# Performance work log

Hardware: AMD Instinct MI355X
Metric: run time of the kernel (lower is better)

The kernel has to match this reference:

```python
import jax, jax.numpy as jnp
import numpy as np

N_NODES = 1_000_000
N_EDGES = 4_000_000  # knn_k = 4
N_GRAPHS = 1024
HIDDEN = 64
N_FEAT = 4


def setup_inputs() -> dict:
    key = jax.random.key(0)
    k0, k1, k2, k3, k4 = jax.random.split(key, 5)
    x = jax.random.normal(k0, (N_NODES, N_FEAT), dtype=jnp.float32)
    edge_index = jax.random.randint(k1, (2, N_EDGES), 0, N_NODES, dtype=jnp.int64)
    batch = jnp.sort(jax.random.randint(k2, (N_NODES,), 0, N_GRAPHS, dtype=jnp.int64))
    W1 = jax.random.normal(k3, (N_FEAT, HIDDEN), dtype=jnp.float32) * 0.5
    b1 = jnp.zeros((HIDDEN,), dtype=jnp.float32)
    W2 = jax.random.normal(k4, (HIDDEN, 1), dtype=jnp.float32) * 0.1
    b2 = jnp.zeros((1,), dtype=jnp.float32)
    return {"x": x, "W1": W1, "b1": b1, "W2": W2, "b2": b2,
            "edge_index": edge_index, "batch": batch}


def gcn_conv(x, edge_index, W, b):
    # PyG GCNConv: linear transform, add self-loops, sym-normalize, scatter-add.
    n = x.shape[0]
    h = x @ W  # [N, 64]
    loop = jnp.arange(n, dtype=edge_index.dtype)
    row = jnp.concatenate([edge_index[0], loop])  # source j
    col = jnp.concatenate([edge_index[1], loop])  # target i
    deg = jax.ops.segment_sum(jnp.ones_like(col, dtype=h.dtype), col, num_segments=n)
    dis = jnp.where(deg > 0, jax.lax.rsqrt(jnp.maximum(deg, 1.0)), 0.0)
    norm = dis[row] * dis[col]  # [E+N]
    out = jax.ops.segment_sum(h[row] * norm[:, None], col, num_segments=n)
    return out + b


def reference(x, W1, b1, W2, b2, edge_index, batch):
    h = gcn_conv(x, edge_index, W1, b1)          # [N, 64]
    h = jax.nn.elu(h)                            # ELU activation
    pooled = jax.ops.segment_sum(h, batch, num_segments=N_GRAPHS)  # global_add_pool
    return pooled @ W2 + b2                      # [G, 1]
```

## Files before the change

kernel.cpp:

```cpp
#include <hip/hip_runtime.h>
#include <hip/hip_fp16.h>

#define N_NODES 1000000
#define N_EDGES 4000000
#define N_GRAPHS 1024
#define HIDDEN 64

#define G1 250
#define T1 512
#define EPB (N_EDGES / G1)
#define EPB4 (EPB / 4)
#define BSHIFT 10
#define BSIZE 1024
#define NBK 1024
#define NBUCK ((N_NODES + BSIZE - 1) / BSIZE)

typedef int   vi4 __attribute__((ext_vector_type(4)));
typedef unsigned vu4 __attribute__((ext_vector_type(4)));
typedef float vf4 __attribute__((ext_vector_type(4)));

__device__ __forceinline__ int4 nt_int4(const int4* p) {
    vi4 v = __builtin_nontemporal_load((const vi4*)p);
    return make_int4(v.x, v.y, v.z, v.w);
}
__device__ __forceinline__ uint4 nt_uint4(const uint4* p) {
    vu4 v = __builtin_nontemporal_load((const vu4*)p);
    return make_uint4(v.x, v.y, v.z, v.w);
}
__device__ __forceinline__ float4 nt_float4(const float4* p) {
    vf4 v = __builtin_nontemporal_load((const vf4*)p);
    return make_float4(v.x, v.y, v.z, v.w);
}

__global__ __launch_bounds__(T1) void k_hist(const int4* __restrict__ col4,
                                             int* __restrict__ part,
                                             float* __restrict__ out,
                                             const float* __restrict__ b2) {
    __shared__ int h[NBK];
    int t = threadIdx.x, blk = blockIdx.x;
    for (int i = t; i < NBK; i += T1) h[i] = 0;
    int gid = blk * T1 + t;
    if (gid < N_GRAPHS) out[gid] = b2[0];
    __syncthreads();
    int b0 = blk * EPB4;
    for (int i = t; i < EPB4; i += T1) {
        int4 c = nt_int4(col4 + b0 + i);
        atomicAdd(&h[((unsigned)c.x) >> BSHIFT], 1);
        atomicAdd(&h[((unsigned)c.y) >> BSHIFT], 1);
        atomicAdd(&h[((unsigned)c.z) >> BSHIFT], 1);
        atomicAdd(&h[((unsigned)c.w) >> BSHIFT], 1);
    }
    __syncthreads();
    for (int i = t; i < NBK; i += T1) part[blk * NBK + i] = h[i];
}

__global__ __launch_bounds__(256) void k_colscan(int* __restrict__ part,
                                                 int* __restrict__ ecnt) {
    int b = blockIdx.x;
    int t = threadIdx.x;
    __shared__ int a[256];
    int v = (t < G1) ? part[t * NBK + b] : 0;
    a[t] = v;
    __syncthreads();
    for (int o = 1; o < 256; o <<= 1) {
        int u = (t >= o) ? a[t - o] : 0;
        __syncthreads();
        a[t] += u;
        __syncthreads();
    }
    if (t < G1) part[t * NBK + b] = a[t] - v;
    if (t == 255) ecnt[b] = a[255];
}

__global__ __launch_bounds__(NBK) void k_bscan(const int* __restrict__ ecnt,
                                               int* __restrict__ ebase) {
    __shared__ int sc[NBK];
    int b = threadIdx.x;
    int run4 = (ecnt[b] + 3) & ~3;
    sc[b] = run4;
    __syncthreads();
    for (int o = 1; o < NBK; o <<= 1) {
        int v = (b >= o) ? sc[b - o] : 0;
        __syncthreads();
        sc[b] += v;
        __syncthreads();
    }
    ebase[b] = sc[b] - run4;
}

__global__ __launch_bounds__(T1) void k_part(const int4* __restrict__ row4,
                                             const int4* __restrict__ col4,
                                             const int* __restrict__ part,
                                             const int* __restrict__ ebase,
                                             unsigned* __restrict__ epair) {
    __shared__ int cur[NBK];
    int t = threadIdx.x, blk = blockIdx.x;
    for (int i = t; i < NBK; i += T1) cur[i] = part[blk * NBK + i] + ebase[i];
    __syncthreads();
    int b0 = blk * EPB4;
    for (int i = t; i < EPB4; i += T1) {
        int4 c = nt_int4(col4 + b0 + i);
        int4 r = nt_int4(row4 + b0 + i);
        int cc[4] = {c.x, c.y, c.z, c.w};
        int rr[4] = {r.x, r.y, r.z, r.w};
        #pragma unroll
        for (int k = 0; k < 4; ++k) {
            int b = ((unsigned)cc[k]) >> BSHIFT;
            int pos = atomicAdd(&cur[b], 1);
            epair[pos] = ((unsigned)(cc[k] & (BSIZE - 1)) << 20) | (unsigned)rr[k];
        }
    }
}

__global__ __launch_bounds__(512) void k_deg2(const unsigned* __restrict__ epair,
                                              const int* __restrict__ ebase,
                                              const int* __restrict__ ecnt,
                                              const float4* __restrict__ x,
                                              float* __restrict__ dis,
                                              uint2* __restrict__ xdh) {
    __shared__ int deg[BSIZE];
    int t = threadIdx.x, b = blockIdx.x;
    for (int i = t; i < BSIZE; i += 512) deg[i] = 1;
    __syncthreads();
    int ne = ecnt[b];
    const unsigned* ep = epair + ebase[b];
    int ne4 = ne & ~3;
    for (int i = 4 * t; i < ne4; i += 2048) {
        uint4 u = nt_uint4((const uint4*)(ep + i));
        atomicAdd(&deg[u.x >> 20], 1);
        atomicAdd(&deg[u.y >> 20], 1);
        atomicAdd(&deg[u.z >> 20], 1);
        atomicAdd(&deg[u.w >> 20], 1);
    }
    for (int i = ne4 + t; i < ne; i += 512) atomicAdd(&deg[ep[i] >> 20], 1);
    __syncthreads();
    int n0 = b << BSHIFT;
    for (int i = t; i < BSIZE; i += 512) {
        int node = n0 + i;
        if (node < N_NODES) {
            float d = rsqrtf((float)deg[i]);
            dis[node] = d;
            float4 xv = nt_float4(x + node);
            __half2 h01 = __floats2half2_rn(xv.x * d, xv.y * d);
            __half2 h23 = __floats2half2_rn(xv.z * d, xv.w * d);
            uint2 pk;
            pk.x = *(unsigned*)&h01;
            pk.y = *(unsigned*)&h23;
            xdh[node] = pk;
        }
    }
}

__device__ __forceinline__ void acc_edge(unsigned u, uint2 p, float* sf) {
    int loc = u >> 20;
    __half2 h01 = *(__half2*)&p.x;
    __half2 h23 = *(__half2*)&p.y;
    float2 f01 = __half22float2(h01);
    float2 f23 = __half22float2(h23);
    float* sp = sf + loc * 5;
    atomicAdd(sp + 0, f01.x);
    atomicAdd(sp + 1, f01.y);
    atomicAdd(sp + 2, f23.x);
    atomicAdd(sp + 3, f23.y);
}

__global__ __launch_bounds__(512) void k_accF(const unsigned* __restrict__ epair,
                                              const int* __restrict__ ebase,
                                              const int* __restrict__ ecnt,
                                              const uint2* __restrict__ xdh,
                                              const float* __restrict__ dis,
                                              const int* __restrict__ batch,
                                              const float* __restrict__ W1,
                                              const float* __restrict__ b1,
                                              const float* __restrict__ W2,
                                              float* __restrict__ out) {
    __shared__ float sf[BSIZE * 5];
    int t = threadIdx.x, b = blockIdx.x;
    for (int i = t; i < BSIZE * 5; i += 512) sf[i] = 0.f;
    __syncthreads();
    int ne = ecnt[b];
    const unsigned* ep = epair + ebase[b];
    int ne8 = ne & ~7;
    for (int i = 8 * t; i < ne8; i += 4096) {
        uint4 q0 = nt_uint4((const uint4*)(ep + i));
        uint4 q1 = nt_uint4((const uint4*)(ep + i + 4));
        uint2 p0 = xdh[q0.x & 0xFFFFFu];
        uint2 p1 = xdh[q0.y & 0xFFFFFu];
        uint2 p2 = xdh[q0.z & 0xFFFFFu];
        uint2 p3 = xdh[q0.w & 0xFFFFFu];
        uint2 p4 = xdh[q1.x & 0xFFFFFu];
        uint2 p5 = xdh[q1.y & 0xFFFFFu];
        uint2 p6 = xdh[q1.z & 0xFFFFFu];
        uint2 p7 = xdh[q1.w & 0xFFFFFu];
        acc_edge(q0.x, p0, sf);
        acc_edge(q0.y, p1, sf);
        acc_edge(q0.z, p2, sf);
        acc_edge(q0.w, p3, sf);
        acc_edge(q1.x, p4, sf);
        acc_edge(q1.y, p5, sf);
        acc_edge(q1.z, p6, sf);
        acc_edge(q1.w, p7, sf);
    }
    for (int i = ne8 + t; i < ne; i += 512) {
        unsigned u = ep[i];
        acc_edge(u, xdh[u & 0xFFFFFu], sf);
    }
    __syncthreads();
    int n0 = b << BSHIFT;
    #pragma unroll
    for (int k = 0; k < BSIZE / 512; ++k) {
        int ln = t + k * 512;
        int node = n0 + ln;
        bool valid = node < N_NODES;
        float acc = 0.f;
        int g = -1;
        if (valid) {
            const float* sp = sf + ln * 5;
            uint2 p = xdh[node];
            __half2 h01 = *(__half2*)&p.x;
            __half2 h23 = *(__half2*)&p.y;
            float2 f01 = __half22float2(h01);
            float2 f23 = __half22float2(h23);
            float d = dis[node];
            float u0 = d * (sp[0] + f01.x);
            float u1 = d * (sp[1] + f01.y);
            float u2 = d * (sp[2] + f23.x);
            float u3 = d * (sp[3] + f23.y);
            g = batch[node];
            #pragma unroll
            for (int kk = 0; kk < HIDDEN; ++kk) {
                float tt = fmaf(u0, W1[kk],
                           fmaf(u1, W1[HIDDEN + kk],
                           fmaf(u2, W1[2 * HIDDEN + kk],
                           fmaf(u3, W1[3 * HIDDEN + kk], b1[kk]))));
                float h = tt > 0.f ? tt : (__expf(tt) - 1.f);
                acc = fmaf(h, W2[kk], acc);
            }
        }
        unsigned long long rem = __ballot(valid);
        while (rem) {
            int leader = __ffsll(rem) - 1;
            int gl = __shfl(g, leader);
            bool mine = valid && (g == gl);
            unsigned long long mask = __ballot(mine);
            float v = mine ? acc : 0.f;
            #pragma unroll
            for (int o = 32; o; o >>= 1) v += __shfl_xor(v, o);
            if ((int)(t & 63) == leader) unsafeAtomicAdd(&out[gl], v);
            rem &= ~mask;
        }
    }
}

__global__ __launch_bounds__(256) void k_init(int* __restrict__ deg, float4* __restrict__ s,
                                              float* __restrict__ out, const float* __restrict__ b2) {
    int i = blockIdx.x * blockDim.x + threadIdx.x;
    if (i < N_NODES) { deg[i] = 1; s[i] = make_float4(0.f, 0.f, 0.f, 0.f); }
    if (i < N_GRAPHS) out[i] = b2[0];
}
__global__ __launch_bounds__(256) void k_deg(const int* __restrict__ col, int* __restrict__ deg) {
    int e = blockIdx.x * blockDim.x + threadIdx.x;
    if (e < N_EDGES) atomicAdd(&deg[col[e]], 1);
}
__global__ __launch_bounds__(256) void k_dis(const int* __restrict__ deg, float* __restrict__ dis) {
    int i = blockIdx.x * blockDim.x + threadIdx.x;
    if (i < N_NODES) dis[i] = rsqrtf((float)deg[i]);
}
__global__ __launch_bounds__(256) void k_scatter(const int* __restrict__ row, const int* __restrict__ col,
                                                 const float4* __restrict__ x, const float* __restrict__ dis,
                                                 float* __restrict__ s) {
    int e = blockIdx.x * blockDim.x + threadIdx.x;
    if (e >= N_EDGES) return;
    int j = row[e], i = col[e];
    float dj = dis[j];
    float4 xj = x[j];
    float* sp = s + 4ll * (long long)i;
    unsafeAtomicAdd(sp + 0, xj.x * dj);
    unsafeAtomicAdd(sp + 1, xj.y * dj);
    unsafeAtomicAdd(sp + 2, xj.z * dj);
    unsafeAtomicAdd(sp + 3, xj.w * dj);
}
__global__ __launch_bounds__(256) void k_node(const float4* __restrict__ x, const float4* __restrict__ s,
                                              const float* __restrict__ dis, const int* __restrict__ batch,
                                              const float* __restrict__ W1, const float* __restrict__ b1,
                                              const float* __restrict__ W2, float* __restrict__ out) {
    int n = blockIdx.x * blockDim.x + threadIdx.x;
    bool valid = n < N_NODES;
    float acc = 0.f; int g = -1;
    if (valid) {
        float4 xn = x[n], sn = s[n];
        float di = dis[n], inv = di * di;
        float u0 = di * sn.x + inv * xn.x, u1 = di * sn.y + inv * xn.y;
        float u2 = di * sn.z + inv * xn.z, u3 = di * sn.w + inv * xn.w;
        g = batch[n];
        #pragma unroll
        for (int k = 0; k < HIDDEN; ++k) {
            float t = fmaf(u0, W1[k], fmaf(u1, W1[HIDDEN + k],
                      fmaf(u2, W1[2 * HIDDEN + k], fmaf(u3, W1[3 * HIDDEN + k], b1[k]))));
            float h = t > 0.f ? t : expm1f(t);
            acc = fmaf(h, W2[k], acc);
        }
    }
    unsigned long long rem = __ballot(valid);
    while (rem) {
        int leader = __ffsll(rem) - 1;
        int gl = __shfl(g, leader);
        bool mine = valid && (g == gl);
        unsigned long long mask = __ballot(mine);
        float v = mine ? acc : 0.f;
        #pragma unroll
        for (int o = 32; o; o >>= 1) v += __shfl_xor(v, o);
        if ((int)(threadIdx.x & 63) == leader) unsafeAtomicAdd(&out[gl], v);
        rem &= ~mask;
    }
}

extern "C" void kernel_launch(void* const* d_in, const int* in_sizes, int n_in,
                              void* d_out, int out_size, void* d_ws, size_t ws_size,
                              hipStream_t stream) {
    const float* x   = (const float*)d_in[0];
    const float* W1  = (const float*)d_in[1];
    const float* b1  = (const float*)d_in[2];
    const float* W2  = (const float*)d_in[3];
    const float* b2  = (const float*)d_in[4];
    const int*   ei  = (const int*)d_in[5];
    const int*   bat = (const int*)d_in[6];
    float* out = (float*)d_out;

    const int* row = ei;
    const int* col = ei + N_EDGES;
    char* ws = (char*)d_ws;

    size_t o_ep   = 0;
    size_t o_xdh  = o_ep + (size_t)(N_EDGES + 4 * NBK) * 4;
    size_t o_dis  = o_xdh + (size_t)N_NODES * 8;
    size_t o_part = o_dis + (size_t)N_NODES * 4;
    size_t o_eb   = o_part + (size_t)G1 * NBK * 4;
    size_t o_ec   = o_eb + NBK * 4;
    size_t need   = o_ec + NBK * 4;

    if (ws_size >= need) {
        unsigned* epair = (unsigned*)(ws + o_ep);
        uint2*    xdh   = (uint2*)(ws + o_xdh);
        float*    dis   = (float*)(ws + o_dis);
        int*      part  = (int*)(ws + o_part);
        int*      ebase = (int*)(ws + o_eb);
        int*      ecnt  = (int*)(ws + o_ec);

        k_hist<<<G1, T1, 0, stream>>>((const int4*)col, part, out, b2);
        k_colscan<<<NBK, 256, 0, stream>>>(part, ecnt);
        k_bscan<<<1, NBK, 0, stream>>>(ecnt, ebase);
        k_part<<<G1, T1, 0, stream>>>((const int4*)row, (const int4*)col, part, ebase, epair);
        k_deg2<<<NBUCK, 512, 0, stream>>>(epair, ebase, ecnt, (const float4*)x, dis, xdh);
        k_accF<<<NBUCK, 512, 0, stream>>>(epair, ebase, ecnt, xdh, dis, bat, W1, b1, W2, out);
    } else {
        int nb_n = (N_NODES + 255) / 256;
        int nb_e = (N_EDGES + 255) / 256;
        int*    deg = (int*)(ws);
        float*  dis = (float*)(ws + (size_t)N_NODES * 4);
        float*  s   = (float*)(ws + (size_t)N_NODES * 8);
        float4* s4  = (float4*)s;
        k_init<<<nb_n, 256, 0, stream>>>(deg, s4, out, b2);
        k_deg<<<nb_e, 256, 0, stream>>>(col, deg);
        k_dis<<<nb_n, 256, 0, stream>>>(deg, dis);
        k_scatter<<<nb_e, 256, 0, stream>>>(row, col, (const float4*)x, dis, s);
        k_node<<<nb_n, 256, 0, stream>>>((const float4*)x, s4, dis, bat, W1, b1, W2, out);
    }
}
```

Measured before the change: 189.8 us.

## Double bucket size, split each bucket by source half, separate MLP kernel

Buckets grow from 1024 to 2048 target nodes. Within each bucket, edges are also sorted by the top bit of the source index, so the gather from xdh in the accumulation phase touches one half of the node array at a time. This is meant to improve L2 locality. The accumulation kernel now runs with 1024 threads and writes per-node sums to a new float4 buffer. A separate k_mlp kernel then does the per-node MLP and graph pooling. The split adds one launch and an extra 16 MB write and read, and deg2 drops the nontemporal x load.

```diff
diff --git a/kernel.cpp b/kernel.cpp
--- a/kernel.cpp
+++ b/kernel.cpp
@@ -10,14 +10,15 @@
 #define T1 512
 #define EPB (N_EDGES / G1)
 #define EPB4 (EPB / 4)
-#define BSHIFT 10
-#define BSIZE 1024
-#define NBK 1024
+#define BSHIFT 11
+#define BSIZE 2048
+#define NBKT 512
+#define NKEY 1024
 #define NBUCK ((N_NODES + BSIZE - 1) / BSIZE)
-
-typedef int   vi4 __attribute__((ext_vector_type(4)));
+#define HALFBIT 19
+
+typedef int      vi4 __attribute__((ext_vector_type(4)));
 typedef unsigned vu4 __attribute__((ext_vector_type(4)));
-typedef float vf4 __attribute__((ext_vector_type(4)));
 
 __device__ __forceinline__ int4 nt_int4(const int4* p) {
     vi4 v = __builtin_nontemporal_load((const vi4*)p);
@@ -27,39 +28,37 @@
     vu4 v = __builtin_nontemporal_load((const vu4*)p);
     return make_uint4(v.x, v.y, v.z, v.w);
 }
-__device__ __forceinline__ float4 nt_float4(const float4* p) {
-    vf4 v = __builtin_nontemporal_load((const vf4*)p);
-    return make_float4(v.x, v.y, v.z, v.w);
-}
 
 __global__ __launch_bounds__(T1) void k_hist(const int4* __restrict__ col4,
+                                             const int4* __restrict__ row4,
                                              int* __restrict__ part,
                                              float* __restrict__ out,
                                              const float* __restrict__ b2) {
-    __shared__ int h[NBK];
+    __shared__ int h[NKEY];
     int t = threadIdx.x, blk = blockIdx.x;
-    for (int i = t; i < NBK; i += T1) h[i] = 0;
+    for (int i = t; i < NKEY; i += T1) h[i] = 0;
     int gid = blk * T1 + t;
     if (gid < N_GRAPHS) out[gid] = b2[0];
     __syncthreads();
     int b0 = blk * EPB4;
     for (int i = t; i < EPB4; i += T1) {
         int4 c = nt_int4(col4 + b0 + i);
-        atomicAdd(&h[((unsigned)c.x) >> BSHIFT], 1);
-        atomicAdd(&h[((unsigned)c.y) >> BSHIFT], 1);
-        atomicAdd(&h[((unsigned)c.z) >> BSHIFT], 1);
-        atomicAdd(&h[((unsigned)c.w) >> BSHIFT], 1);
-    }
-    __syncthreads();
-    for (int i = t; i < NBK; i += T1) part[blk * NBK + i] = h[i];
+        int4 r = nt_int4(row4 + b0 + i);
+        atomicAdd(&h[((((unsigned)c.x) >> BSHIFT) << 1) | (((unsigned)r.x) >> HALFBIT)], 1);
+        atomicAdd(&h[((((unsigned)c.y) >> BSHIFT) << 1) | (((unsigned)r.y) >> HALFBIT)], 1);
+        atomicAdd(&h[((((unsigned)c.z) >> BSHIFT) << 1) | (((unsigned)r.z) >> HALFBIT)], 1);
+        atomicAdd(&h[((((unsigned)c.w) >> BSHIFT) << 1) | (((unsigned)r.w) >> HALFBIT)], 1);
+    }
+    __syncthreads();
+    for (int i = t; i < NKEY; i += T1) part[blk * NKEY + i] = h[i];
 }
 
 __global__ __launch_bounds__(256) void k_colscan(int* __restrict__ part,
-                                                 int* __restrict__ ecnt) {
+                                                 int* __restrict__ keycnt) {
     int b = blockIdx.x;
     int t = threadIdx.x;
     __shared__ int a[256];
-    int v = (t < G1) ? part[t * NBK + b] : 0;
+    int v = (t < G1) ? part[t * NKEY + b] : 0;
     a[t] = v;
     __syncthreads();
     for (int o = 1; o < 256; o <<= 1) {
@@ -68,34 +67,45 @@
         a[t] += u;
         __syncthreads();
     }
-    if (t < G1) part[t * NBK + b] = a[t] - v;
-    if (t == 255) ecnt[b] = a[255];
-}
-
-__global__ __launch_bounds__(NBK) void k_bscan(const int* __restrict__ ecnt,
-                                               int* __restrict__ ebase) {
-    __shared__ int sc[NBK];
+    if (t < G1) part[t * NKEY + b] = a[t] - v;
+    if (t == 255) keycnt[b] = a[255];
+}
+
+__global__ __launch_bounds__(NBKT) void k_bscan(const int* __restrict__ keycnt,
+                                                int* __restrict__ keybase,
+                                                int* __restrict__ ebase,
+                                                int* __restrict__ ecnt,
+                                                int* __restrict__ esplit) {
+    __shared__ int sc[NBKT];
     int b = threadIdx.x;
-    int run4 = (ecnt[b] + 3) & ~3;
-    sc[b] = run4;
-    __syncthreads();
-    for (int o = 1; o < NBK; o <<= 1) {
+    int kc0 = keycnt[2 * b];
+    int kc1 = keycnt[2 * b + 1];
+    int tot = kc0 + kc1;
+    int tot4 = (tot + 3) & ~3;
+    sc[b] = tot4;
+    __syncthreads();
+    for (int o = 1; o < NBKT; o <<= 1) {
         int v = (b >= o) ? sc[b - o] : 0;
         __syncthreads();
         sc[b] += v;
         __syncthreads();
     }
-    ebase[b] = sc[b] - run4;
+    int base = sc[b] - tot4;
+    keybase[2 * b] = base;
+    keybase[2 * b + 1] = base + kc0;
+    ebase[b] = base;
+    ecnt[b] = tot;
+    esplit[b] = kc0;
 }
 
 __global__ __launch_bounds__(T1) void k_part(const int4* __restrict__ row4,
                                              const int4* __restrict__ col4,
                                              const int* __restrict__ part,
-                                             const int* __restrict__ ebase,
+                                             const int* __restrict__ keybase,
                                              unsigned* __restrict__ epair) {
-    __shared__ int cur[NBK];
+    __shared__ int cur[NKEY];
     int t = threadIdx.x, blk = blockIdx.x;
-    for (int i = t; i < NBK; i += T1) cur[i] = part[blk * NBK + i] + ebase[i];
+    for (int i = t; i < NKEY; i += T1) cur[i] = part[blk * NKEY + i] + keybase[i];
     __syncthreads();
     int b0 = blk * EPB4;
     for (int i = t; i < EPB4; i += T1) {
@@ -105,9 +115,10 @@
         int rr[4] = {r.x, r.y, r.z, r.w};
         #pragma unroll
         for (int k = 0; k < 4; ++k) {
-            int b = ((unsigned)cc[k]) >> BSHIFT;
-            int pos = atomicAdd(&cur[b], 1);
-            epair[pos] = ((unsigned)(cc[k] & (BSIZE - 1)) << 20) | (unsigned)rr[k];
+            unsigned cu = (unsigned)cc[k], ru = (unsigned)rr[k];
+            int key = ((cu >> BSHIFT) << 1) | (ru >> HALFBIT);
+            int pos = atomicAdd(&cur[key], 1);
+            epair[pos] = ((cu & (BSIZE - 1)) << 20) | ru;
         }
     }
 }
@@ -140,7 +151,7 @@
         if (node < N_NODES) {
             float d = rsqrtf((float)deg[i]);
             dis[node] = d;
-            float4 xv = nt_float4(x + node);
+            float4 xv = x[node];
             __half2 h01 = __floats2half2_rn(xv.x * d, xv.y * d);
             __half2 h23 = __floats2half2_rn(xv.z * d, xv.w * d);
             uint2 pk;
@@ -164,91 +175,97 @@
     atomicAdd(sp + 3, f23.y);
 }
 
-__global__ __launch_bounds__(512) void k_accF(const unsigned* __restrict__ epair,
+__global__ __launch_bounds__(1024) void k_acc(const unsigned* __restrict__ epair,
                                               const int* __restrict__ ebase,
                                               const int* __restrict__ ecnt,
+                                              const int* __restrict__ esplit,
                                               const uint2* __restrict__ xdh,
-                                              const float* __restrict__ dis,
-                                              const int* __restrict__ batch,
-                                              const float* __restrict__ W1,
-                                              const float* __restrict__ b1,
-                                              const float* __restrict__ W2,
-                                              float* __restrict__ out) {
+                                              float4* __restrict__ sbuf) {
     __shared__ float sf[BSIZE * 5];
     int t = threadIdx.x, b = blockIdx.x;
-    for (int i = t; i < BSIZE * 5; i += 512) sf[i] = 0.f;
+    for (int i = t; i < BSIZE * 5; i += 1024) sf[i] = 0.f;
     __syncthreads();
     int ne = ecnt[b];
+    int sp_ = esplit[b];
     const unsigned* ep = epair + ebase[b];
-    int ne8 = ne & ~7;
-    for (int i = 8 * t; i < ne8; i += 4096) {
-        uint4 q0 = nt_uint4((const uint4*)(ep + i));
-        uint4 q1 = nt_uint4((const uint4*)(ep + i + 4));
-        uint2 p0 = xdh[q0.x & 0xFFFFFu];
-        uint2 p1 = xdh[q0.y & 0xFFFFFu];
-        uint2 p2 = xdh[q0.z & 0xFFFFFu];
-        uint2 p3 = xdh[q0.w & 0xFFFFFu];
-        uint2 p4 = xdh[q1.x & 0xFFFFFu];
-        uint2 p5 = xdh[q1.y & 0xFFFFFu];
-        uint2 p6 = xdh[q1.z & 0xFFFFFu];
-        uint2 p7 = xdh[q1.w & 0xFFFFFu];
-        acc_edge(q0.x, p0, sf);
-        acc_edge(q0.y, p1, sf);
-        acc_edge(q0.z, p2, sf);
-        acc_edge(q0.w, p3, sf);
-        acc_edge(q1.x, p4, sf);
-        acc_edge(q1.y, p5, sf);
-        acc_edge(q1.z, p6, sf);
-        acc_edge(q1.w, p7, sf);
-    }
-    for (int i = ne8 + t; i < ne; i += 512) {
-        unsigned u = ep[i];
-        acc_edge(u, xdh[u & 0xFFFFFu], sf);
+    #pragma unroll
+    for (int ph = 0; ph < 2; ++ph) {
+        int s = ph ? sp_ : 0;
+        int e = ph ? ne : sp_;
+        int i = s + 4 * t;
+        for (; i + 3 < e; i += 4096) {
+            unsigned u0 = ep[i], u1 = ep[i + 1], u2 = ep[i + 2], u3 = ep[i + 3];
+            uint2 p0 = xdh[u0 & 0xFFFFFu];
+            uint2 p1 = xdh[u1 & 0xFFFFFu];
+            uint2 p2 = xdh[u2 & 0xFFFFFu];
+            uint2 p3 = xdh[u3 & 0xFFFFFu];
+            acc_edge(u0, p0, sf);
+            acc_edge(u1, p1, sf);
+            acc_edge(u2, p2, sf);
+            acc_edge(u3, p3, sf);
+        }
+        for (; i < e; ++i) {
+            unsigned u = ep[i];
+            acc_edge(u, xdh[u & 0xFFFFFu], sf);
+        }
     }
     __syncthreads();
     int n0 = b << BSHIFT;
-    #pragma unroll
-    for (int k = 0; k < BSIZE / 512; ++k) {
-        int ln = t + k * 512;
-        int node = n0 + ln;
-        bool valid = node < N_NODES;
-        float acc = 0.f;
-        int g = -1;
-        if (valid) {
-            const float* sp = sf + ln * 5;
-            uint2 p = xdh[node];
-            __half2 h01 = *(__half2*)&p.x;
-            __half2 h23 = *(__half2*)&p.y;
-            float2 f01 = __half22float2(h01);
-            float2 f23 = __half22float2(h23);
-            float d = dis[node];
-            float u0 = d * (sp[0] + f01.x);
-            float u1 = d * (sp[1] + f01.y);
-            float u2 = d * (sp[2] + f23.x);
-            float u3 = d * (sp[3] + f23.y);
-            g = batch[node];
-            #pragma unroll
-            for (int kk = 0; kk < HIDDEN; ++kk) {
-                float tt = fmaf(u0, W1[kk],
-                           fmaf(u1, W1[HIDDEN + kk],
-                           fmaf(u2, W1[2 * HIDDEN + kk],
-                           fmaf(u3, W1[3 * HIDDEN + kk], b1[kk]))));
-                float h = tt > 0.f ? tt : (__expf(tt) - 1.f);
-                acc = fmaf(h, W2[kk], acc);
-            }
-        }
-        unsigned long long rem = __ballot(valid);
-        while (rem) {
-            int leader = __ffsll(rem) - 1;
-            int gl = __shfl(g, leader);
-            bool mine = valid && (g == gl);
-            unsigned long long mask = __ballot(mine);
-            float v = mine ? acc : 0.f;
-            #pragma unroll
-            for (int o = 32; o; o >>= 1) v += __shfl_xor(v, o);
-            if ((int)(t & 63) == leader) unsafeAtomicAdd(&out[gl], v);
-            rem &= ~mask;
-        }
+    for (int i = t; i < BSIZE; i += 1024) {
+        int node = n0 + i;
+        if (node < N_NODES) {
+            const float* q = sf + i * 5;
+            sbuf[node] = make_float4(q[0], q[1], q[2], q[3]);
+        }
+    }
+}
+
+__global__ __launch_bounds__(256) void k_mlp(const float4* __restrict__ sbuf,
+                                             const uint2* __restrict__ xdh,
+                                             const float* __restrict__ dis,
+                                             const int* __restrict__ batch,
+                                             const float* __restrict__ W1,
+                                             const float* __restrict__ b1,
+                                             const float* __restrict__ W2,
+                                             float* __restrict__ out) {
+    int n = blockIdx.x * blockDim.x + threadIdx.x;
+    bool valid = n < N_NODES;
+    float acc = 0.f;
+    int g = -1;
+    if (valid) {
+        float4 sv = sbuf[n];
+        uint2 p = xdh[n];
+        __half2 h01 = *(__half2*)&p.x;
+        __half2 h23 = *(__half2*)&p.y;
+        float2 f01 = __half22float2(h01);
+        float2 f23 = __half22float2(h23);
+        float d = dis[n];
+        float u0 = d * (sv.x + f01.x);
+        float u1 = d * (sv.y + f01.y);
+        float u2 = d * (sv.z + f23.x);
+        float u3 = d * (sv.w + f23.y);
+        g = batch[n];
+        #pragma unroll
+        for (int k = 0; k < HIDDEN; ++k) {
+            float t = fmaf(u0, W1[k],
+                      fmaf(u1, W1[HIDDEN + k],
+                      fmaf(u2, W1[2 * HIDDEN + k],
+                      fmaf(u3, W1[3 * HIDDEN + k], b1[k]))));
+            float h = t > 0.f ? t : (__expf(t) - 1.f);
+            acc = fmaf(h, W2[k], acc);
+        }
+    }
+    unsigned long long rem = __ballot(valid);
+    while (rem) {
+        int leader = __ffsll(rem) - 1;
+        int gl = __shfl(g, leader);
+        bool mine = valid && (g == gl);
+        unsigned long long mask = __ballot(mine);
+        float v = mine ? acc : 0.f;
+        #pragma unroll
+        for (int o = 32; o; o >>= 1) v += __shfl_xor(v, o);
+        if ((int)(threadIdx.x & 63) == leader) unsafeAtomicAdd(&out[gl], v);
+        rem &= ~mask;
     }
 }
 
@@ -332,27 +349,36 @@
     char* ws = (char*)d_ws;
 
     size_t o_ep   = 0;
-    size_t o_xdh  = o_ep + (size_t)(N_EDGES + 4 * NBK) * 4;
+    size_t o_sb   = o_ep + (size_t)(N_EDGES + 4 * NBKT) * 4;
+    size_t o_xdh  = o_sb + (size_t)N_NODES * 16;
     size_t o_dis  = o_xdh + (size_t)N_NODES * 8;
     size_t o_part = o_dis + (size_t)N_NODES * 4;
-    size_t o_eb   = o_part + (size_t)G1 * NBK * 4;
-    size_t o_ec   = o_eb + NBK * 4;
-    size_t need   = o_ec + NBK * 4;
+    size_t o_kc   = o_part + (size_t)G1 * NKEY * 4;
+    size_t o_kb   = o_kc + NKEY * 4;
+    size_t o_eb   = o_kb + NKEY * 4;
+    size_t o_ec   = o_eb + NBKT * 4;
+    size_t o_es   = o_ec + NBKT * 4;
+    size_t need   = o_es + NBKT * 4;
 
     if (ws_size >= need) {
-        unsigned* epair = (unsigned*)(ws + o_ep);
-        uint2*    xdh   = (uint2*)(ws + o_xdh);
-        float*    dis   = (float*)(ws + o_dis);
-        int*      part  = (int*)(ws + o_part);
-        int*      ebase = (int*)(ws + o_eb);
-        int*      ecnt  = (int*)(ws + o_ec);
-
-        k_hist<<<G1, T1, 0, stream>>>((const int4*)col, part, out, b2);
-        k_colscan<<<NBK, 256, 0, stream>>>(part, ecnt);
-        k_bscan<<<1, NBK, 0, stream>>>(ecnt, ebase);
-        k_part<<<G1, T1, 0, stream>>>((const int4*)row, (const int4*)col, part, ebase, epair);
+        unsigned* epair   = (unsigned*)(ws + o_ep);
+        float4*   sbuf    = (float4*)(ws + o_sb);
+        uint2*    xdh     = (uint2*)(ws + o_xdh);
+        float*    dis     = (float*)(ws + o_dis);
+        int*      part    = (int*)(ws + o_part);
+        int*      keycnt  = (int*)(ws + o_kc);
+        int*      keybase = (int*)(ws + o_kb);
+        int*      ebase   = (int*)(ws + o_eb);
+        int*      ecnt    = (int*)(ws + o_ec);
+        int*      esplit  = (int*)(ws + o_es);
+
+        k_hist<<<G1, T1, 0, stream>>>((const int4*)col, (const int4*)row, part, out, b2);
+        k_colscan<<<NKEY, 256, 0, stream>>>(part, keycnt);
+        k_bscan<<<1, NBKT, 0, stream>>>(keycnt, keybase, ebase, ecnt, esplit);
+        k_part<<<G1, T1, 0, stream>>>((const int4*)row, (const int4*)col, part, keybase, epair);
         k_deg2<<<NBUCK, 512, 0, stream>>>(epair, ebase, ecnt, (const float4*)x, dis, xdh);
-        k_accF<<<NBUCK, 512, 0, stream>>>(epair, ebase, ecnt, xdh, dis, bat, W1, b1, W2, out);
+        k_acc<<<NBUCK, 1024, 0, stream>>>(epair, ebase, ecnt, esplit, xdh, sbuf);
+        k_mlp<<<(N_NODES + 255) / 256, 256, 0, stream>>>(sbuf, xdh, dis, bat, W1, b1, W2, out);
     } else {
         int nb_n = (N_NODES + 255) / 256;
         int nb_e = (N_EDGES + 255) / 256;
```

Result: slower. 209.0 us (+10.1%).
